# Kernel optimization log

Hardware: AMD Instinct MI355X
Metric: run time of the kernel (lower is better)

Reference implementation:

```python
import jax, jax.numpy as jnp
import numpy as np

B, N, DIM = 8, 1024, 768
H, HD = 12, 64
INNER = H * HD
SCALE = HD ** -0.5


def setup_inputs() -> dict:
    key = jax.random.key(0)
    ks = jax.random.split(key, 6)
    return {
        "x": jax.random.normal(ks[0], (B, N, DIM), dtype=jnp.float32),
        "w_qkv": jax.random.normal(ks[1], (DIM, 3 * INNER), dtype=jnp.float32) * 0.02,
        "b_qkv": jax.random.normal(ks[2], (3 * INNER,), dtype=jnp.float32) * 0.02,
        "reattn_weights": jax.random.normal(ks[3], (H, HD, HD), dtype=jnp.float32),
        "w_out": jax.random.normal(ks[4], (INNER, DIM), dtype=jnp.float32) * 0.02,
        "b_out": jax.random.normal(ks[5], (DIM,), dtype=jnp.float32) * 0.02,
    }


def reference(x, w_qkv, b_qkv, reattn_weights, w_out, b_out):
    b, n, _ = x.shape
    qkv = x @ w_qkv + b_qkv  # [b, n, 3*inner]
    q, k, v = jnp.split(qkv, 3, axis=-1)
    # 'b n (h d) -> b h n d'
    def to_heads(t):
        return t.reshape(b, n, H, HD).transpose(0, 2, 1, 3)
    q, k, v = to_heads(q), to_heads(k), to_heads(v)
    dots = jnp.einsum('bhid,bhjd->bhij', q, k) * SCALE
    attn = jax.nn.softmax(dots, axis=-1)
    # einsum 'b h i j, h d e -> b h i j' sums d,e out: per-head scalar scale
    head_scale = reattn_weights.sum(axis=(-1, -2))  # [h]
    attn = attn * head_scale[None, :, None, None]
    out = jnp.einsum('bhij,bhjd->bhid', attn, v)
    out = out.transpose(0, 2, 1, 3).reshape(b, n, INNER)  # 'b h n d -> b n (h d)'
    return out @ w_out + b_out
```

## Files before the change

kernel.cpp:

```cpp
#include <hip/hip_runtime.h>

constexpr int Bn   = 8;
constexpr int Nn   = 1024;
constexpr int DIMn = 768;
constexpr int Hn   = 12;
constexpr int HDn  = 64;
constexpr int INNERn = Hn * HDn;
constexpr int QKVCOLS = 3 * INNERn;
constexpr int Mrows = Bn * Nn;
constexpr float QSCL = 0.18033688011112042f;

typedef float f32x4 __attribute__((ext_vector_type(4)));
typedef __bf16 bf16x8 __attribute__((ext_vector_type(8)));
typedef __bf16 bf16x4 __attribute__((ext_vector_type(4)));

static __device__ __forceinline__ float fexp2(float x) {
#if __has_builtin(__builtin_amdgcn_exp2f)
    return __builtin_amdgcn_exp2f(x);
#else
    return exp2f(x);
#endif
}

static __device__ __forceinline__ void gload16(const void* g, void* l) {
    __builtin_amdgcn_global_load_lds(
        (const __attribute__((address_space(1))) unsigned int*)g,
        (__attribute__((address_space(3))) unsigned int*)l, 16, 0, 0);
}

__global__ __launch_bounds__(256) void prep_kernel(
    const float* __restrict__ wqkv, const float* __restrict__ wout,
    const float* __restrict__ rw,
    __bf16* __restrict__ wqkvT, __bf16* __restrict__ woutT,
    float* __restrict__ hs)
{
    __shared__ float Ls[64][68];
    __shared__ float red[256];
    const int bx = blockIdx.x;
    const int t = threadIdx.x;

    if (bx >= 48) {
        if (blockIdx.y != 0) return;
        int h = bx - 48;
        const float* p = rw + (size_t)h * (HDn * HDn);
        float s = 0.f;
        for (int i = t; i < HDn * HDn; i += 256) s += p[i];
        red[t] = s;
        __syncthreads();
        #pragma unroll
        for (int off = 128; off > 0; off >>= 1) {
            if (t < off) red[t] += red[t + off];
            __syncthreads();
        }
        if (t == 0) hs[h] = red[0];
        return;
    }

    const float* w;  __bf16* wT;  int N, n0;
    if (bx < 36) { w = wqkv; wT = wqkvT; N = QKVCOLS; n0 = bx * 64; }
    else         { w = wout; wT = woutT; N = INNERn;  n0 = (bx - 36) * 64; }
    int k0 = blockIdx.y * 64;
    int cc = t & 15, rr = t >> 4;
    #pragma unroll
    for (int it = 0; it < 4; ++it) {
        int row = rr + it * 16;
        float4 v = *(const float4*)(w + (size_t)(k0 + row) * N + n0 + cc * 4);
        *(float4*)(&Ls[row][cc * 4]) = v;
    }
    __syncthreads();
    #pragma unroll
    for (int it = 0; it < 4; ++it) {
        int nr = rr + it * 16;
        bf16x4 o;
        #pragma unroll
        for (int i = 0; i < 4; ++i) o[i] = (__bf16)Ls[cc * 4 + i][nr];
        *(bf16x4*)(wT + (size_t)(n0 + nr) * 768 + k0 + cc * 4) = o;
    }
}

template<int EPI, int AF32>
__global__ __launch_bounds__(256) void gemm_bf16_kernel(
    const void* __restrict__ Ap, const __bf16* __restrict__ BT,
    const float* __restrict__ bias,
    __bf16* __restrict__ qb, __bf16* __restrict__ kb, __bf16* __restrict__ vt,
    float* __restrict__ outp)
{
    constexpr int K = 768;
    __shared__ __attribute__((aligned(16))) char AsRaw[AF32 ? 32768 : 16384];
    __shared__ __attribute__((aligned(16))) __bf16 Bs[128][64];

    const float*  A32 = (const float*)Ap;
    const __bf16* A16 = (const __bf16*)Ap;
    float*  As32 = (float*)AsRaw;
    __bf16* As16 = (__bf16*)AsRaw;

    const int tid = threadIdx.x;
    const int lane = tid & 63, w = tid >> 6;
    const int g = lane >> 4, l16 = lane & 15;
    const int wm = (w >> 1) * 64, wn = (w & 1) * 64;
    const int bid = blockIdx.x;
    const int m0 = (bid & 63) * 128;
    const int n0 = (bid >> 6) * 128;

    f32x4 acc[4][4] = {};

    for (int kt = 0; kt < K; kt += 64) {
        __syncthreads();
        if (AF32) {
            int lr = lane >> 4, sl = lane & 15;
            #pragma unroll
            for (int i = 0; i < 8; ++i) {
                int rbase = w * 32 + i * 4;
                int row = rbase + lr;
                gload16(A32 + (size_t)(m0 + row) * K + kt + ((sl ^ (row & 15)) << 2),
                        As32 + rbase * 64);
            }
        } else {
            int lr = lane >> 3, sl = lane & 7;
            #pragma unroll
            for (int i = 0; i < 4; ++i) {
                int rbase = w * 32 + i * 8;
                int row = rbase + lr;
                gload16(A16 + (size_t)(m0 + row) * K + kt + ((sl ^ (row & 7)) << 3),
                        As16 + rbase * 64);
            }
        }
        {
            int lr = lane >> 3, sl = lane & 7;
            #pragma unroll
            for (int i = 0; i < 4; ++i) {
                int rbase = w * 32 + i * 8;
                int row = rbase + lr;
                gload16(BT + (size_t)(n0 + row) * K + kt + ((sl ^ (row & 7)) << 3),
                        &Bs[rbase][0]);
            }
        }
        __syncthreads();

        #pragma unroll
        for (int s = 0; s < 2; ++s) {
            bf16x8 af[4], bfr[4];
            #pragma unroll
            for (int f = 0; f < 4; ++f) {
                int ar = wm + f * 16 + l16;
                if (AF32) {
                    const float* base = As32 + ar * 64;
                    f32x4 va0 = *(const f32x4*)(base + (((s * 8 + g * 2 + 0) ^ l16) << 2));
                    f32x4 va1 = *(const f32x4*)(base + (((s * 8 + g * 2 + 1) ^ l16) << 2));
                    af[f] = bf16x8{ (__bf16)va0[0], (__bf16)va0[1], (__bf16)va0[2], (__bf16)va0[3],
                                    (__bf16)va1[0], (__bf16)va1[1], (__bf16)va1[2], (__bf16)va1[3] };
                } else {
                    af[f] = *(const bf16x8*)(As16 + ar * 64 + ((s * 4 + g) ^ (ar & 7)) * 8);
                }
                int br = wn + f * 16 + l16;
                bfr[f] = *(const bf16x8*)(&Bs[br][((s * 4 + g) ^ (br & 7)) * 8]);
            }
            #pragma unroll
            for (int fa = 0; fa < 4; ++fa)
                #pragma unroll
                for (int fb = 0; fb < 4; ++fb)
                    acc[fa][fb] = __builtin_amdgcn_mfma_f32_16x16x32_bf16(
                        af[fa], bfr[fb], acc[fa][fb], 0, 0, 0);
        }
    }

    #pragma unroll
    for (int fa = 0; fa < 4; ++fa) {
        #pragma unroll
        for (int fb = 0; fb < 4; ++fb) {
            int n = n0 + wn + fb * 16 + l16;
            float bn = bias[n];
            float v0 = acc[fa][fb][0] + bn;
            float v1 = acc[fa][fb][1] + bn;
            float v2 = acc[fa][fb][2] + bn;
            float v3 = acc[fa][fb][3] + bn;
            int mbase = m0 + wm + fa * 16 + g * 4;
            if (EPI == 0) {
                int which = n / INNERn;
                int rem = n - which * INNERn;
                int hh = rem >> 6, d = rem & 63;
                int bb = mbase >> 10;
                int nn = mbase & 1023;
                size_t bh = (size_t)bb * Hn + hh;
                if (which == 2) {
                    bf16x4 o = { (__bf16)v0, (__bf16)v1, (__bf16)v2, (__bf16)v3 };
                    *(bf16x4*)(vt + (bh * 64 + d) * Nn + nn) = o;
                } else {
                    float sc = (which == 0) ? QSCL : 1.0f;
                    __bf16* dst = (which == 0) ? qb : kb;
                    size_t base = ((bh * Nn + nn) << 6) + d;
                    dst[base]       = (__bf16)(v0 * sc);
                    dst[base + 64]  = (__bf16)(v1 * sc);
                    dst[base + 128] = (__bf16)(v2 * sc);
                    dst[base + 192] = (__bf16)(v3 * sc);
                }
            } else {
                outp[(size_t)(mbase + 0) * INNERn + n] = v0;
                outp[(size_t)(mbase + 1) * INNERn + n] = v1;
                outp[(size_t)(mbase + 2) * INNERn + n] = v2;
                outp[(size_t)(mbase + 3) * INNERn + n] = v3;
            }
        }
    }
}

__global__ __launch_bounds__(256) void attn_mfma_kernel(
    const __bf16* __restrict__ qb, const __bf16* __restrict__ kb,
    const __bf16* __restrict__ vT, const float* __restrict__ hs,
    __bf16* __restrict__ ao)
{
    __shared__ __attribute__((aligned(16))) __bf16 Ks[2][64][64];
    __shared__ __attribute__((aligned(16))) __bf16 Vs[2][64][64];

    const int tid = threadIdx.x;
    const int lane = tid & 63, w = tid >> 6;
    const int g = lane >> 4, l16 = lane & 15;
    const int bid = blockIdx.x;
    const int bh = bid % 96;
    const int qt = bid / 96;
    const int b = bh / Hn, h = bh - b * Hn;

    const __bf16* Qp = qb + ((size_t)bh * Nn + qt * 128 + w * 16) * 64;
    const __bf16* Kp = kb + (size_t)bh * Nn * 64;
    const __bf16* Vp = vT + (size_t)bh * 64 * Nn;

    const int srl = lane >> 3;
    const int ssl = lane & 7;

    bf16x8 qf[2][2];
    #pragma unroll
    for (int t = 0; t < 2; ++t)
        #pragma unroll
        for (int s = 0; s < 2; ++s)
            qf[t][s] = *(const bf16x8*)(Qp + t * 64 * 64 + (size_t)l16 * 64 + s * 32 + g * 8);

    float l0 = 0.f, l1 = 0.f;
    f32x4 oacc0[4] = {}, oacc1[4] = {};

    #pragma unroll
    for (int i = 0; i < 2; ++i) {
        int row = w * 16 + i * 8 + srl;
        gload16(Kp + (size_t)row * 64 + ((ssl ^ (row & 7)) << 3),
                &Ks[0][w * 16 + i * 8][0]);
        gload16(Vp + (size_t)row * Nn + ((ssl ^ (row & 7)) << 3),
                &Vs[0][w * 16 + i * 8][0]);
    }
    __syncthreads();

    int cur = 0;
    for (int jt = 0; jt < Nn / 64; ++jt) {
        if (jt < Nn / 64 - 1) {
            const __bf16* kbase = Kp + (size_t)(jt + 1) * 64 * 64;
            const __bf16* vbase = Vp + (size_t)(jt + 1) * 64;
            #pragma unroll
            for (int i = 0; i < 2; ++i) {
                int row = w * 16 + i * 8 + srl;
                gload16(kbase + (size_t)row * 64 + ((ssl ^ (row & 7)) << 3),
                        &Ks[cur ^ 1][w * 16 + i * 8][0]);
                gload16(vbase + (size_t)row * Nn + ((ssl ^ (row & 7)) << 3),
                        &Vs[cur ^ 1][w * 16 + i * 8][0]);
            }
        }

        f32x4 st0[4] = {}, st1[4] = {};
        #pragma unroll
        for (int s = 0; s < 2; ++s) {
            #pragma unroll
            for (int jf = 0; jf < 4; ++jf) {
                bf16x8 kf = *(const bf16x8*)(
                    &Ks[cur][jf * 16 + l16][((s * 4 + g) ^ (l16 & 7)) * 8]);
                st0[jf] = __builtin_amdgcn_mfma_f32_16x16x32_bf16(kf, qf[0][s], st0[jf], 0, 0, 0);
                st1[jf] = __builtin_amdgcn_mfma_f32_16x16x32_bf16(kf, qf[1][s], st1[jf], 0, 0, 0);
            }
        }

        #pragma unroll
        for (int f = 0; f < 4; ++f)
            #pragma unroll
            for (int r = 0; r < 4; ++r) {
                float p0 = fexp2(st0[f][r]); st0[f][r] = p0; l0 += p0;
                float p1 = fexp2(st1[f][r]); st1[f][r] = p1; l1 += p1;
            }

        bf16x8 pa0[2], pa1[2];
        #pragma unroll
        for (int s = 0; s < 2; ++s) {
            pa0[s] = bf16x8{ (__bf16)st0[2*s][0], (__bf16)st0[2*s][1],
                             (__bf16)st0[2*s][2], (__bf16)st0[2*s][3],
                             (__bf16)st0[2*s+1][0], (__bf16)st0[2*s+1][1],
                             (__bf16)st0[2*s+1][2], (__bf16)st0[2*s+1][3] };
            pa1[s] = bf16x8{ (__bf16)st1[2*s][0], (__bf16)st1[2*s][1],
                             (__bf16)st1[2*s][2], (__bf16)st1[2*s][3],
                             (__bf16)st1[2*s+1][0], (__bf16)st1[2*s+1][1],
                             (__bf16)st1[2*s+1][2], (__bf16)st1[2*s+1][3] };
        }

        #pragma unroll
        for (int s = 0; s < 2; ++s) {
            #pragma unroll
            for (int df = 0; df < 4; ++df) {
                const __bf16* vrow = &Vs[cur][df * 16 + l16][0];
                int c0 = s * 32 + g * 4;
                int i0 = ((c0 >> 3) ^ (l16 & 7)) * 8 + (c0 & 7);
                int c1 = c0 + 16;
                int i1 = ((c1 >> 3) ^ (l16 & 7)) * 8 + (c1 & 7);
                bf16x4 v0 = *(const bf16x4*)(vrow + i0);
                bf16x4 v1 = *(const bf16x4*)(vrow + i1);
                bf16x8 bv = { v0[0], v0[1], v0[2], v0[3], v1[0], v1[1], v1[2], v1[3] };
                oacc0[df] = __builtin_amdgcn_mfma_f32_16x16x32_bf16(pa0[s], bv, oacc0[df], 0, 0, 0);
                oacc1[df] = __builtin_amdgcn_mfma_f32_16x16x32_bf16(pa1[s], bv, oacc1[df], 0, 0, 0);
            }
        }

        __syncthreads();
        cur ^= 1;
    }

    l0 += __shfl_xor(l0, 16);  l0 += __shfl_xor(l0, 32);
    l1 += __shfl_xor(l1, 16);  l1 += __shfl_xor(l1, 32);
    float linv0 = hs[h] / l0;
    float linv1 = hs[h] / l1;

    #pragma unroll
    for (int reg = 0; reg < 4; ++reg) {
        float li0 = __shfl(linv0, 20 * g + reg);
        float li1 = __shfl(linv1, 20 * g + reg);
        int q0 = qt * 128 + w * 16 + g * 4 + reg;
        #pragma unroll
        for (int df = 0; df < 4; ++df) {
            ao[((size_t)b * Nn + q0) * INNERn + h * 64 + df * 16 + l16] =
                (__bf16)(oacc0[df][reg] * li0);
            ao[((size_t)b * Nn + q0 + 64) * INNERn + h * 64 + df * 16 + l16] =
                (__bf16)(oacc1[df][reg] * li1);
        }
    }
}

extern "C" void kernel_launch(void* const* d_in, const int* in_sizes, int n_in,
                              void* d_out, int out_size, void* d_ws, size_t ws_size,
                              hipStream_t stream)
{
    const float* x    = (const float*)d_in[0];
    const float* wqkv = (const float*)d_in[1];
    const float* bqkv = (const float*)d_in[2];
    const float* rw   = (const float*)d_in[3];
    const float* wout = (const float*)d_in[4];
    const float* bout = (const float*)d_in[5];
    float* out = (float*)d_out;
    (void)in_sizes; (void)n_in; (void)out_size; (void)ws_size;

    char* ws = (char*)d_ws;
    size_t off = 0;
    auto alloc = [&](size_t bytes) -> char* {
        char* p = ws + off; off += (bytes + 255) & ~(size_t)255; return p;
    };
    const size_t tsz = (size_t)Mrows * INNERn;
    float*  hsb   = (float*) alloc(Hn * 4);
    __bf16* wqkvT = (__bf16*)alloc((size_t)QKVCOLS * DIMn * 2);
    __bf16* woutT = (__bf16*)alloc((size_t)INNERn * DIMn * 2);
    __bf16* qbuf  = (__bf16*)alloc(tsz * 2);
    __bf16* kbuf  = (__bf16*)alloc(tsz * 2);
    __bf16* vTb   = (__bf16*)alloc(tsz * 2);
    __bf16* aob   = (__bf16*)alloc(tsz * 2);

    prep_kernel<<<dim3(60, 12), dim3(256), 0, stream>>>(
        wqkv, wout, rw, wqkvT, woutT, hsb);

    gemm_bf16_kernel<0, 1><<<dim3((QKVCOLS / 128) * (Mrows / 128)), dim3(256), 0, stream>>>(
        x, wqkvT, bqkv, qbuf, kbuf, vTb, nullptr);

    attn_mfma_kernel<<<dim3((Nn / 128) * Bn * Hn), dim3(256), 0, stream>>>(
        qbuf, kbuf, vTb, hsb, aob);

    gemm_bf16_kernel<1, 0><<<dim3((INNERn / 128) * (Mrows / 128)), dim3(256), 0, stream>>>(
        aob, woutT, bout, nullptr, nullptr, nullptr, out);
}
```

Baseline: 122.8 us.

## Permute V^T layout for single 16-byte LDS reads and compute row sums via MFMA

The QKV projection epilogue now writes V^T with a permuted column order inside each 64-key block, so the attention kernel can fetch each PV B-operand with one 16-byte LDS load instead of two 8-byte loads plus a repack. The softmax denominator is now accumulated by an extra MFMA against a vector of ones, replacing per-element scalar adds and the cross-lane shuffles at the end. This cuts VALU and LDS instruction count in the inner loop, at the cost of two extra MFMAs per step and a denominator built from bf16-rounded probabilities.

```diff
diff --git a/kernel.cpp b/kernel.cpp
--- a/kernel.cpp
+++ b/kernel.cpp
@@ -183,8 +183,11 @@
                 int nn = mbase & 1023;
                 size_t bh = (size_t)bb * Hn + hh;
                 if (which == 2) {
+                    int nn0 = nn & ~63;
+                    int u = nn & 63;
+                    int p = (u & 32) + (((u & 15) >> 2) << 3) + (((u >> 4) & 1) << 2);
                     bf16x4 o = { (__bf16)v0, (__bf16)v1, (__bf16)v2, (__bf16)v3 };
-                    *(bf16x4*)(vt + (bh * 64 + d) * Nn + nn) = o;
+                    *(bf16x4*)(vt + (bh * 64 + d) * Nn + nn0 + p) = o;
                 } else {
                     float sc = (which == 0) ? QSCL : 1.0f;
                     __bf16* dst = (which == 0) ? qb : kb;
@@ -227,6 +230,9 @@
     const int srl = lane >> 3;
     const int ssl = lane & 7;
 
+    const __bf16 one1 = (__bf16)1.0f;
+    const bf16x8 vones = { one1, one1, one1, one1, one1, one1, one1, one1 };
+
     bf16x8 qf[2][2];
     #pragma unroll
     for (int t = 0; t < 2; ++t)
@@ -234,8 +240,8 @@
         for (int s = 0; s < 2; ++s)
             qf[t][s] = *(const bf16x8*)(Qp + t * 64 * 64 + (size_t)l16 * 64 + s * 32 + g * 8);
 
-    float l0 = 0.f, l1 = 0.f;
     f32x4 oacc0[4] = {}, oacc1[4] = {};
+    f32x4 lacc0 = {}, lacc1 = {};
 
     #pragma unroll
     for (int i = 0; i < 2; ++i) {
@@ -278,8 +284,8 @@
         for (int f = 0; f < 4; ++f)
             #pragma unroll
             for (int r = 0; r < 4; ++r) {
-                float p0 = fexp2(st0[f][r]); st0[f][r] = p0; l0 += p0;
-                float p1 = fexp2(st1[f][r]); st1[f][r] = p1; l1 += p1;
+                st0[f][r] = fexp2(st0[f][r]);
+                st1[f][r] = fexp2(st1[f][r]);
             }
 
         bf16x8 pa0[2], pa1[2];
@@ -297,16 +303,12 @@
 
         #pragma unroll
         for (int s = 0; s < 2; ++s) {
+            lacc0 = __builtin_amdgcn_mfma_f32_16x16x32_bf16(pa0[s], vones, lacc0, 0, 0, 0);
+            lacc1 = __builtin_amdgcn_mfma_f32_16x16x32_bf16(pa1[s], vones, lacc1, 0, 0, 0);
             #pragma unroll
             for (int df = 0; df < 4; ++df) {
-                const __bf16* vrow = &Vs[cur][df * 16 + l16][0];
-                int c0 = s * 32 + g * 4;
-                int i0 = ((c0 >> 3) ^ (l16 & 7)) * 8 + (c0 & 7);
-                int c1 = c0 + 16;
-                int i1 = ((c1 >> 3) ^ (l16 & 7)) * 8 + (c1 & 7);
-                bf16x4 v0 = *(const bf16x4*)(vrow + i0);
-                bf16x4 v1 = *(const bf16x4*)(vrow + i1);
-                bf16x8 bv = { v0[0], v0[1], v0[2], v0[3], v1[0], v1[1], v1[2], v1[3] };
+                bf16x8 bv = *(const bf16x8*)(
+                    &Vs[cur][df * 16 + l16][((s * 4 + g) ^ (l16 & 7)) * 8]);
                 oacc0[df] = __builtin_amdgcn_mfma_f32_16x16x32_bf16(pa0[s], bv, oacc0[df], 0, 0, 0);
                 oacc1[df] = __builtin_amdgcn_mfma_f32_16x16x32_bf16(pa1[s], bv, oacc1[df], 0, 0, 0);
             }
@@ -316,15 +318,11 @@
         cur ^= 1;
     }
 
-    l0 += __shfl_xor(l0, 16);  l0 += __shfl_xor(l0, 32);
-    l1 += __shfl_xor(l1, 16);  l1 += __shfl_xor(l1, 32);
-    float linv0 = hs[h] / l0;
-    float linv1 = hs[h] / l1;
-
+    const float hscale = hs[h];
     #pragma unroll
     for (int reg = 0; reg < 4; ++reg) {
-        float li0 = __shfl(linv0, 20 * g + reg);
-        float li1 = __shfl(linv1, 20 * g + reg);
+        float li0 = hscale / lacc0[reg];
+        float li1 = hscale / lacc1[reg];
         int q0 = qt * 128 + w * 16 + g * 4 + reg;
         #pragma unroll
         for (int df = 0; df < 4; ++df) {
```

After: 112.2 us (median of 3 runs). 1.09x faster.
